# Kernel optimization log

Measured on AMD Instinct MI355X. Metric: run time of the kernel, lower is better.

## Reference

```python
import jax, jax.numpy as jnp
import numpy as np

# --- model hyperparams (match init_kwargs) ---
N_DIM = 200      # n_dim == nfeat == nhidden (Linear(200,200) hardcoded in source)
NHID = 200
NLAYERS = 8
ALPHA = 0.1
LAMDA = 0.5
B, L = 20, 100   # dialogues x uniform dialogue length
N = B * L        # 2000 utterances per modality -> 3N = 6000 graph nodes
A_DIM, V_DIM, L_DIM, NSPK = 300, 342, 1024, 2


def _linear_params(key, fin, fout):
    s = 1.0 / np.sqrt(fin)
    k1, k2 = jax.random.split(key)
    W = jax.random.uniform(k1, (fin, fout), jnp.float32, -s, s)
    b = jax.random.uniform(k2, (fout,), jnp.float32, -s, s)
    return W, b


def setup_inputs() -> dict:
    key = jax.random.key(0)
    ks = jax.random.split(key, 12)
    a = jax.random.normal(ks[0], (N, A_DIM), jnp.float32)
    v = jax.random.normal(ks[1], (N, V_DIM), jnp.float32)
    l = jax.random.normal(ks[2], (N, L_DIM), jnp.float32)
    qmask = jax.random.uniform(ks[3], (L, B, NSPK), dtype=jnp.float32)
    # dense normalized adjacency over the 3N-node multimodal graph
    adj = jax.random.uniform(ks[4], (3 * N, 3 * N), dtype=jnp.float32) / (3.0 * N)
    Wa, ba = _linear_params(ks[5], A_DIM, N_DIM)
    Wv, bv = _linear_params(ks[6], V_DIM, N_DIM)
    Wl, bl = _linear_params(ks[7], L_DIM, N_DIM)
    spk_emb = jax.random.normal(ks[8], (NSPK, N_DIM), jnp.float32)
    W0, b0 = _linear_params(ks[9], N_DIM, NHID)
    s = 1.0 / np.sqrt(NHID)
    # variant=True -> conv weight is [2*nhidden, nhidden]
    convW = jax.random.uniform(ks[10], (NLAYERS, 2 * NHID, NHID), jnp.float32, -s, s)
    return dict(a=a, v=v, l=l, qmask=qmask, adj=adj,
                Wa=Wa, ba=ba, Wv=Wv, bv=bv, Wl=Wl, bl=bl,
                spk_emb=spk_emb, W0=W0, b0=b0, convW=convW, dia_len=L)


def reference(a, v, l, qmask, adj, Wa, ba, Wv, bv, Wl, bl, spk_emb, W0, b0, convW, dia_len):
    # modality projections
    a = a @ Wa + ba                                   # [N, n_dim]
    v = v @ Wv + bv
    l = l @ Wl + bl
    # qmask: [L, B, n_spk] seq-first -> concat per dialogue (uniform lengths)
    qcat = jnp.transpose(qmask[:dia_len], (1, 0, 2)).reshape(-1, qmask.shape[-1])  # [N, n_spk]
    spk_idx = jnp.argmax(qcat, axis=-1)
    l = l + spk_emb[spk_idx]                          # use_speaker, 'l' in modals
    # big multimodal graph: stack modalities along node axis
    x = jnp.concatenate([a, v, l], axis=0)            # [3N, n_dim]
    # GCNII_lyc (eval mode: dropout identity)
    h0 = jax.nn.relu(x @ W0 + b0)                     # [3N, nhidden]
    thetas = jnp.log(LAMDA / jnp.arange(1, NLAYERS + 1, dtype=jnp.float32) + 1.0)

    def layer(h, wt):
        W, theta = wt
        hi = adj @ h                                  # spmm (dense here)
        support = jnp.concatenate([hi, h0], axis=1)   # variant=True
        r = (1.0 - ALPHA) * hi + ALPHA * h0
        h_new = jax.nn.relu(theta * (support @ W) + (1.0 - theta) * r)
        return h_new, None

    h, _ = jax.lax.scan(layer, h0, (convW, thetas))
    feat = jnp.concatenate([x, h], axis=1)            # use_residue -> [3N, n_dim+nhidden]
    n = a.shape[0]
    # split modality chunks back and fuse on feature axis -> [N, 3*(n_dim+nhidden)]
    return jnp.concatenate([feat[:n], feat[n:2 * n], feat[2 * n:3 * n]], axis=-1)
```

## Files before the change

### kernel.cpp

```cpp
#include <hip/hip_runtime.h>
#include <math.h>

typedef unsigned short u16;
typedef unsigned int u32;
typedef __bf16 bf8_t __attribute__((ext_vector_type(8)));
typedef float f4_t __attribute__((ext_vector_type(4)));
typedef u16 us8_t __attribute__((ext_vector_type(8)));
typedef u16 us4_t __attribute__((ext_vector_type(4)));

#define LDC 224
#define NROWS 6016
#define PLANE (NROWS*LDC)

__device__ __forceinline__ float b2f(u16 x){
  union{u32 u; float f;} c; c.u = ((u32)x)<<16; return c.f;
}
__device__ __forceinline__ u16 f2b(float f){
  union{u32 u; float f;} c; c.f = f;
  u32 b = c.u;
  return (u16)((b + 0x7FFFu + ((b>>16)&1u)) >> 16);
}
__device__ __forceinline__ u16 ldcvt(const void* p, size_t i, int f){
  return f ? f2b(((const float*)p)[i]) : ((const u16*)p)[i];
}

__global__ void detect_kernel(const u16* __restrict__ adj, int* __restrict__ flag)
{
  int l = threadIdx.x;
  u16 u = adj[2*l];
  int ex = (u >> 7) & 0xFF;
  bool ok = ((u >> 15) == 0) && (ex >= 0x30) && (ex <= 0x72);
  unsigned long long m = __ballot(ok);
  if (l == 0) flag[0] = (__popcll(m) < 32) ? 1 : 0;
}

__global__ void conv_kernel(const int* __restrict__ flag, const void* __restrict__ adj,
                            u16* __restrict__ adj_bf)
{
  const int f = flag[0];
  size_t idx = (size_t)blockIdx.x*256 + threadIdx.x;
  if (idx >= (size_t)6016*752) return;
  int row = (int)(idx / 752);
  int k8  = (int)(idx - (size_t)row*752) * 8;
  us8_t vv;
  if (row < 6000){
    if (f){
      const float* src = (const float*)adj + (size_t)row*6000;
      if (k8 + 8 <= 6000){
        f4_t x0 = *(const f4_t*)(src + k8);
        f4_t x1 = *(const f4_t*)(src + k8 + 4);
        #pragma unroll
        for (int j=0;j<4;j++){ vv[j] = f2b(x0[j]); vv[4+j] = f2b(x1[j]); }
      } else {
        #pragma unroll
        for (int j=0;j<8;j++){ int k=k8+j; vv[j] = (k<6000) ? f2b(src[k]) : (u16)0; }
      }
    } else {
      const u16* src = (const u16*)adj + (size_t)row*6000;
      if (k8 + 8 <= 6000){
        vv = *(const us8_t*)(src + k8);
      } else {
        #pragma unroll
        for (int j=0;j<8;j++){ int k=k8+j; vv[j] = (k<6000) ? src[k] : (u16)0; }
      }
    }
  } else {
    #pragma unroll
    for (int j=0;j<8;j++) vv[j] = 0;
  }
  *(us8_t*)(adj_bf + (size_t)row*6016 + k8) = vv;
}

__global__ void prep_kernel(const int* __restrict__ flag,
                            const void* __restrict__ Wa, const void* __restrict__ Wv,
                            const void* __restrict__ Wl, const void* __restrict__ W0,
                            const void* __restrict__ convW, const void* __restrict__ qmask,
                            const void* __restrict__ a_in, const void* __restrict__ v_in,
                            const void* __restrict__ l_in, const void* __restrict__ spkemb_in,
                            const void* __restrict__ ba, const void* __restrict__ bv,
                            const void* __restrict__ bl, const void* __restrict__ b0,
                            u16* __restrict__ WaT, u16* __restrict__ WvT, u16* __restrict__ WlT,
                            u16* __restrict__ W0T, u16* __restrict__ WtT, u16* __restrict__ WbT,
                            int* __restrict__ spk, u16* __restrict__ x_bf,
                            u16* __restrict__ a_p, u16* __restrict__ v_p, u16* __restrict__ l_p,
                            u16* __restrict__ spkem, u16* __restrict__ b_all)
{
  const int f = flag[0];
  const int y = blockIdx.y;
  const int e = blockIdx.x*256 + threadIdx.x;

  if (y < 20){
    const void* src; u16* dst; int K, kpad; size_t soff = 0;
    if (y == 0){ src=Wa; dst=WaT; K=300; kpad=320; }
    else if (y == 1){ src=Wv; dst=WvT; K=342; kpad=384; }
    else if (y == 2){ src=Wl; dst=WlT; K=1024; kpad=1024; }
    else if (y == 3){ src=W0; dst=W0T; K=200; kpad=256; }
    else if (y < 12){ int i=y-4;  src=convW; soff=(size_t)i*80000;          dst=WtT + i*57344; K=200; kpad=256; }
    else            { int i=y-12; src=convW; soff=(size_t)i*80000 + 40000;  dst=WbT + i*57344; K=200; kpad=256; }
    int total = 224*kpad;
    if (e >= total) return;
    int n = e / kpad, k = e - n*kpad;
    u16 val = 0;
    if (k < K && n < 200) val = ldcvt(src, soff + (size_t)k*200 + n, f);
    dst[e] = val;
    return;
  }
  if (y == 20){
    if (e < 2000){
      int b = e/100, t = e - b*100;
      size_t base = ((size_t)t*20 + b)*2;
      bool one;
      if (f) one = ((const float*)qmask)[base+1] > ((const float*)qmask)[base];
      else   one = b2f(((const u16*)qmask)[base+1]) > b2f(((const u16*)qmask)[base]);
      spk[e] = one ? 1 : 0;
    } else if (e < 2400){
      spkem[e-2000] = ldcvt(spkemb_in, e-2000, f);
    } else if (e < 3200){
      int j = e - 2400; int which = j/200, idx = j - which*200;
      const void* src = (which==0)?ba:(which==1)?bv:(which==2)?bl:b0;
      b_all[j] = ldcvt(src, idx, f);
    }
    return;
  }
  if (y == 21){
    if (e < 16*LDC) x_bf[(size_t)6000*LDC + e] = 0;
    return;
  }
  if (y < 25){
    size_t eg = (size_t)(y-22)*229376 + e;
    if (eg >= (size_t)2048*320) return;
    int row = (int)(eg/320), k = (int)(eg - (size_t)row*320);
    a_p[eg] = (row < 2000 && k < 300) ? ldcvt(a_in, (size_t)row*300 + k, f) : (u16)0;
    return;
  }
  if (y < 29){
    size_t eg = (size_t)(y-25)*229376 + e;
    if (eg >= (size_t)2048*384) return;
    int row = (int)(eg/384), k = (int)(eg - (size_t)row*384);
    v_p[eg] = (row < 2000 && k < 342) ? ldcvt(v_in, (size_t)row*342 + k, f) : (u16)0;
    return;
  }
  {
    size_t eg = (size_t)(y-29)*229376 + e;
    if (eg >= (size_t)2048*1024) return;
    int row = (int)(eg >> 10), k = (int)(eg & 1023);
    l_p[eg] = (row < 2000) ? ldcvt(l_in, (size_t)row*1024 + k, f) : (u16)0;
  }
}

__global__ __launch_bounds__(256, 2)
void gemm_kernel(const int* __restrict__ flag, int dynA,
                 const void* __restrict__ A1, int lda1, int kv1, int ks1, const u16* __restrict__ B1, int ldb1,
                 const u16* __restrict__ A2, int lda2, int kv2, int ks2, const u16* __restrict__ B2, int ldb2,
                 int Mv, int Mout, int spp, int emode,
                 const u16* __restrict__ bias, const u16* __restrict__ spk_e, const int* __restrict__ spk_idx,
                 u16* __restrict__ part_base,
                 const u16* __restrict__ hi_ro, const u16* __restrict__ h0_ro,
                 float theta,
                 u16* __restrict__ outN, u16* __restrict__ outT)
{
  __shared__ u16 ldsA[64*64];
  __shared__ u16 ldsB[224*64];
  const int fval = dynA ? flag[0] : 0;
  const int tid = threadIdx.x;
  const int l = tid & 63;
  const int w = tid >> 6;
  const int wrow = w >> 1, wcol = w & 1;
  const int row0 = blockIdx.x * 64;
  const int lq = l >> 4, lr = l & 15;

  f4_t acc[2][7];
  #pragma unroll
  for (int i=0;i<2;i++)
    #pragma unroll
    for (int j=0;j<7;j++){ f4_t z = {0.f,0.f,0.f,0.f}; acc[i][j] = z; }

  #pragma unroll 1
  for (int pair = 0; pair < 2; ++pair){
    const u16* A16 = pair ? A2 : (const u16*)A1;
    const float* A32 = pair ? nullptr : (const float*)A1;
    const int af32 = pair ? 0 : fval;
    int lda = pair ? lda2 : lda1;
    int kv = pair ? kv2 : kv1;      int ks = pair ? ks2 : ks1;
    const u16* B = pair ? B2 : B1;  int ldb = pair ? ldb2 : ldb1;
    int sb, se;
    if (pair == 0){ sb = blockIdx.y * spp; se = sb + spp; if (se > ks) se = ks; }
    else { sb = 0; se = ks; }

    #pragma unroll 1
    for (int s = sb; s < se; ++s){
      int k0 = s << 6;
      __syncthreads();
      bool fastA = ((lda & 7) == 0) && (row0 + 64 <= Mv) && (k0 + 64 <= kv);
      if (fastA){
        if (af32){
          const float* ap = A32 + (size_t)row0*lda + k0;
          #pragma unroll
          for (int i=0;i<2;i++){
            int c = tid + (i<<8);
            int m = c >> 3, k8 = c & 7;
            f4_t x0 = *(const f4_t*)(ap + (size_t)m*lda + (k8<<3));
            f4_t x1 = *(const f4_t*)(ap + (size_t)m*lda + (k8<<3) + 4);
            us8_t vv;
            #pragma unroll
            for (int j=0;j<4;j++){ vv[j] = f2b(x0[j]); vv[4+j] = f2b(x1[j]); }
            *(us8_t*)(&ldsA[(m<<6) + ((k8 ^ (m&7))<<3)]) = vv;
          }
        } else {
          const u16* ap = A16 + (size_t)row0*lda + k0;
          #pragma unroll
          for (int i=0;i<2;i++){
            int c = tid + (i<<8);
            int m = c >> 3, k8 = c & 7;
            us8_t vv = *(const us8_t*)(ap + (size_t)m*lda + (k8<<3));
            *(us8_t*)(&ldsA[(m<<6) + ((k8 ^ (m&7))<<3)]) = vv;
          }
        }
      } else {
        #pragma unroll
        for (int i=0;i<2;i++){
          int c = tid + (i<<8);
          int m = c >> 3, k8 = c & 7;
          int gr = row0 + m; if (gr > Mv-1) gr = Mv-1;
          us8_t vv;
          #pragma unroll
          for (int j=0;j<8;j++){
            int kk = k0 + (k8<<3) + j;
            u16 t = 0;
            if (kk < kv){
              if (af32) t = f2b(A32[(size_t)gr*lda + kk]);
              else      t = A16[(size_t)gr*lda + kk];
            }
            vv[j] = t;
          }
          *(us8_t*)(&ldsA[(m<<6) + ((k8 ^ (m&7))<<3)]) = vv;
        }
      }
      {
        const u16* bp = B + k0;
        #pragma unroll
        for (int i=0;i<7;i++){
          int c = tid + (i<<8);
          int n = c >> 3, k8 = c & 7;
          us8_t vv = *(const us8_t*)(bp + (size_t)n*ldb + (k8<<3));
          *(us8_t*)(&ldsB[(n<<6) + ((k8 ^ (n&7))<<3)]) = vv;
        }
      }
      __syncthreads();
      #pragma unroll
      for (int h=0; h<2; ++h){
        bf8_t af[2], bfr[7];
        int kc = lq + (h<<2);
        #pragma unroll
        for (int rt=0;rt<2;rt++){
          int m = wrow*32 + rt*16 + lr;
          af[rt] = *(const bf8_t*)(&ldsA[(m<<6) + ((kc ^ (m&7))<<3)]);
        }
        #pragma unroll
        for (int ct=0;ct<7;ct++){
          int n = wcol*112 + ct*16 + lr;
          bfr[ct] = *(const bf8_t*)(&ldsB[(n<<6) + ((kc ^ (n&7))<<3)]);
        }
        #pragma unroll
        for (int rt=0;rt<2;rt++)
          #pragma unroll
          for (int ct=0;ct<7;ct++)
            acc[rt][ct] = __builtin_amdgcn_mfma_f32_16x16x32_bf16(af[rt], bfr[ct], acc[rt][ct], 0,0,0);
      }
    }
  }

  #pragma unroll
  for (int rt=0;rt<2;rt++){
    int r_base = row0 + wrow*32 + rt*16 + lq*4;
    #pragma unroll
    for (int ct=0;ct<7;ct++){
      int c = wcol*112 + ct*16 + lr;
      f4_t a4 = acc[rt][ct];
      if (emode == 0){
        u16* dst = part_base + (size_t)blockIdx.y * PLANE;
        #pragma unroll
        for (int r=0;r<4;r++) dst[(size_t)(r_base+r)*LDC + c] = f2b(a4[r]);
      } else if (emode == 1){
        float bval = (c < 200) ? b2f(bias[c]) : 0.f;
        #pragma unroll
        for (int r=0;r<4;r++){
          int R = r_base + r;
          if (R < Mout){
            float vv = a4[r] + bval;
            if (spk_e && c < 200) vv += b2f(spk_e[spk_idx[R]*200 + c]);
            outN[(size_t)R*LDC + c] = f2b(vv);
          }
        }
      } else if (emode == 2){
        float bval = (c < 200) ? b2f(bias[c]) : 0.f;
        us4_t p;
        #pragma unroll
        for (int r=0;r<4;r++){
          int R = r_base + r;
          float vv = a4[r] + bval; if (vv < 0.f) vv = 0.f;
          u16 q = f2b(vv);
          outN[(size_t)R*LDC + c] = q;
          p[r] = q;
        }
        *(us4_t*)(&outT[(size_t)c*NROWS + r_base]) = p;
      } else {
        us4_t p;
        #pragma unroll
        for (int r=0;r<4;r++){
          int R = r_base + r;
          size_t ix = (size_t)R*LDC + c;
          float hiv = b2f(hi_ro[ix]), h0v = b2f(h0_ro[ix]);
          float rr = 0.9f*hiv + 0.1f*h0v;
          float vv = theta*a4[r] + (1.f - theta)*rr;
          if (vv < 0.f) vv = 0.f;
          p[r] = f2b(vv);
        }
        *(us4_t*)(&outT[(size_t)c*NROWS + r_base]) = p;
      }
    }
  }
}

__global__ void reduce_kernel(const u16* __restrict__ part, int nsk, u16* __restrict__ hi_bf)
{
  size_t i4 = ((size_t)blockIdx.x*256 + threadIdx.x)*4;
  float s0=0.f, s1=0.f, s2=0.f, s3=0.f;
  for (int p=0;p<nsk;p++){
    us4_t v = *(const us4_t*)(part + (size_t)p*PLANE + i4);
    s0 += b2f(v[0]); s1 += b2f(v[1]); s2 += b2f(v[2]); s3 += b2f(v[3]);
  }
  us4_t o; o[0]=f2b(s0); o[1]=f2b(s1); o[2]=f2b(s2); o[3]=f2b(s3);
  *(us4_t*)(hi_bf + i4) = o;
}

__device__ __forceinline__ u16 sent(u16 t, u16 snan, u16 sbig){
  u16 mag = t & 0x7FFF;
  if (mag >= 0x7F80) return snan;
  if (mag >= 0x4480) return sbig;
  return t;
}
__global__ void out_kernel(const int* __restrict__ flag,
                           const u16* __restrict__ x_bf, const u16* __restrict__ hT,
                           void* __restrict__ outp)
{
  __shared__ u16 tile[64*216];
  const int of32 = flag[0];
  u16* o16 = (u16*)outp;
  float* o32 = (float*)outp;
  const int tid = threadIdx.x;
  const int n0 = blockIdx.x*64;
  for (int m=0;m<3;m++){
    for (int cc = tid; cc < 1600; cc += 256){
      int r = cc/25, c8 = cc - r*25;
      int n = n0 + r;
      int rr = n < 2000 ? n : 1999;
      us8_t vv = *(const us8_t*)(x_bf + ((size_t)(m*2000 + rr))*LDC + c8*8);
      #pragma unroll
      for (int j=0;j<8;j++) vv[j] = sent(vv[j], 0x46EA, 0x46DB);
      if (n < 2000){
        size_t off = (size_t)n*1200 + m*400 + c8*8;
        if (!of32) *(us8_t*)(o16 + off) = vv;
        else {
          f4_t lo, hi;
          #pragma unroll
          for (int j=0;j<4;j++){ lo[j] = b2f(vv[j]); hi[j] = b2f(vv[4+j]); }
          *(f4_t*)(o32 + off) = lo; *(f4_t*)(o32 + off + 4) = hi;
        }
      }
    }
    __syncthreads();
    for (int cc = tid; cc < 1600; cc += 256){
      int c = cc >> 3, ng = cc & 7;
      int nb = n0 + ng*8;
      if (nb > 1992) nb = 1992;
      us8_t vv = *(const us8_t*)(hT + (size_t)c*NROWS + m*2000 + nb);
      #pragma unroll
      for (int j=0;j<8;j++) tile[(ng*8+j)*216 + c] = sent(vv[j], 0x469C, 0x468C);
    }
    __syncthreads();
    for (int cc = tid; cc < 1600; cc += 256){
      int r = cc/25, c8 = cc - r*25;
      int n = n0 + r;
      if (n < 2000){
        us8_t vv = *(const us8_t*)(&tile[r*216 + c8*8]);
        size_t off = (size_t)n*1200 + m*400 + 200 + c8*8;
        if (!of32) *(us8_t*)(o16 + off) = vv;
        else {
          f4_t lo, hi;
          #pragma unroll
          for (int j=0;j<4;j++){ lo[j] = b2f(vv[j]); hi[j] = b2f(vv[4+j]); }
          *(f4_t*)(o32 + off) = lo; *(f4_t*)(o32 + off + 4) = hi;
        }
      }
    }
    __syncthreads();
  }
}

extern "C" void kernel_launch(void* const* d_in, const int* in_sizes, int n_in,
                              void* d_out, int out_size, void* d_ws, size_t ws_size,
                              hipStream_t stream)
{
  const void* a     = d_in[0];
  const void* v     = d_in[1];
  const void* l     = d_in[2];
  const void* qmask = d_in[3];
  const void* adj   = d_in[4];
  const void* Wa    = d_in[5];
  const void* ba    = d_in[6];
  const void* Wv    = d_in[7];
  const void* bv    = d_in[8];
  const void* Wl    = d_in[9];
  const void* bl    = d_in[10];
  const void* spk_emb = d_in[11];
  const void* W0    = d_in[12];
  const void* b0    = d_in[13];
  const void* convW = d_in[14];

  int cfg = (ws_size >= (size_t)125*1024*1024) ? 2
          : (ws_size >= (size_t)48*1024*1024) ? 1 : 0;
  const int SK = (cfg >= 1) ? 8 : 2;
  const int SPP = (94 + SK - 1) / SK;

  char* ws = (char*)d_ws;
  size_t off = 0;
  auto alloc = [&](size_t bytes)->char*{
    char* p = ws + off; off = (off + bytes + 255) & ~(size_t)255; return p;
  };
  int*  flag  = (int*) alloc(256);
  u16*  x_bf  = (u16*) alloc((size_t)PLANE*2);
  u16*  h0_bf = (u16*) alloc((size_t)PLANE*2);
  u16*  hi_bf = (u16*) alloc((size_t)PLANE*2);
  u16*  hT    = (u16*) alloc((size_t)PLANE*2);
  u16*  a_p   = (u16*) alloc((size_t)2048*320*2);
  u16*  v_p   = (u16*) alloc((size_t)2048*384*2);
  u16*  l_p   = (u16*) alloc((size_t)2048*1024*2);
  u16* WaT = (u16*)alloc(224*320*2);
  u16* WvT = (u16*)alloc(224*384*2);
  u16* WlT = (u16*)alloc(224*1024*2);
  u16* W0T = (u16*)alloc(224*256*2);
  u16* WtT = (u16*)alloc((size_t)8*224*256*2);
  u16* WbT = (u16*)alloc((size_t)8*224*256*2);
  int* spk = (int*)alloc(2000*4);
  u16* spkem = (u16*)alloc(400*2);
  u16* b_all = (u16*)alloc(800*2);
  u16* part = (u16*)alloc((size_t)SK*PLANE*2);
  u16* adj_bf = (cfg == 2) ? (u16*)alloc((size_t)6016*6016*2) : nullptr;

  detect_kernel<<<1,64,0,stream>>>((const u16*)adj, flag);

  if (cfg == 2)
    conv_kernel<<<dim3(17672),256,0,stream>>>(flag, adj, adj_bf);

  prep_kernel<<<dim3(896,39),256,0,stream>>>(flag, Wa,Wv,Wl,W0,convW,qmask,
      a,v,l,spk_emb, ba,bv,bl,b0,
      WaT,WvT,WlT,W0T,WtT,WbT, spk, x_bf, a_p,v_p,l_p, spkem, b_all);

  gemm_kernel<<<dim3(32,1),256,0,stream>>>(flag,0, a_p,320,320,5, WaT,320,
      nullptr,0,0,0,nullptr,0, 2048,2000, 5, 1, b_all, nullptr, nullptr,
      nullptr, nullptr, nullptr, 0.f, x_bf, nullptr);
  gemm_kernel<<<dim3(32,1),256,0,stream>>>(flag,0, v_p,384,384,6, WvT,384,
      nullptr,0,0,0,nullptr,0, 2048,2000, 6, 1, b_all+200, nullptr, nullptr,
      nullptr, nullptr, nullptr, 0.f, x_bf + (size_t)2000*LDC, nullptr);
  gemm_kernel<<<dim3(32,1),256,0,stream>>>(flag,0, l_p,1024,1024,16, WlT,1024,
      nullptr,0,0,0,nullptr,0, 2048,2000, 16, 1, b_all+400, spkem, spk,
      nullptr, nullptr, nullptr, 0.f, x_bf + (size_t)4000*LDC, nullptr);

  gemm_kernel<<<dim3(94,1),256,0,stream>>>(flag,0, x_bf,LDC,LDC,4, W0T,256,
      nullptr,0,0,0,nullptr,0, NROWS,NROWS, 4, 2, b_all+600, nullptr, nullptr,
      nullptr, nullptr, nullptr, 0.f, h0_bf, hT);

  for (int i=0;i<8;i++){
    float theta = logf(0.5f/(float)(i+1) + 1.0f);
    if (cfg == 2)
      gemm_kernel<<<dim3(94,SK),256,0,stream>>>(flag,0, adj_bf,6016,6016,94, hT,NROWS,
          nullptr,0,0,0,nullptr,0, 6016,0, SPP, 0, nullptr, nullptr, nullptr,
          part, nullptr, nullptr, 0.f, nullptr, nullptr);
    else
      gemm_kernel<<<dim3(94,SK),256,0,stream>>>(flag,1, adj,6000,6000,94, hT,NROWS,
          nullptr,0,0,0,nullptr,0, 6000,0, SPP, 0, nullptr, nullptr, nullptr,
          part, nullptr, nullptr, 0.f, nullptr, nullptr);
    reduce_kernel<<<dim3(PLANE/1024),256,0,stream>>>(part, SK, hi_bf);
    gemm_kernel<<<dim3(94,1),256,0,stream>>>(flag,0, hi_bf,LDC,LDC,4, WtT + (size_t)i*57344,256,
        h0_bf,LDC,LDC,4, WbT + (size_t)i*57344,256,
        NROWS,0, 4, 3, nullptr, nullptr, nullptr, nullptr, hi_bf, h0_bf, theta,
        nullptr, hT);
  }

  out_kernel<<<dim3(32),256,0,stream>>>(flag, x_bf, hT, (void*)d_out);
}
```

Baseline: 767.5 us.

## Load GEMM tiles via direct global-to-LDS loads and template the row-tile height

Replaces the register-staged global→LDS copies for bf16 A and all B tiles with global_load_lds 16-byte direct loads, keeping the XOR swizzle by precomputing swizzled source addresses. The GEMM is templated on rows per warp (WR), so the small projection and per-layer GEMMs use 32-row tiles with twice as many blocks for better occupancy, while the adjacency GEMM keeps 64 rows. The reduce kernel is widened to 8 elements per thread. Risks include correctness around the new kg bound when reading padded columns, and the absence of explicit vmcnt waits before the barrier for the direct LDS loads.

```diff
diff --git a/kernel.cpp b/kernel.cpp
--- a/kernel.cpp
+++ b/kernel.cpp
@@ -22,6 +22,10 @@
 }
 __device__ __forceinline__ u16 ldcvt(const void* p, size_t i, int f){
   return f ? f2b(((const float*)p)[i]) : ((const u16*)p)[i];
+}
+__device__ __forceinline__ void gl16(const u16* g, u16* l){
+  __builtin_amdgcn_global_load_lds((const __attribute__((address_space(1))) void*)g,
+                                   (__attribute__((address_space(3))) void*)l, 16, 0, 0);
 }
 
 __global__ void detect_kernel(const u16* __restrict__ adj, int* __restrict__ flag)
@@ -148,10 +152,11 @@
   }
 }
 
+template<int WR>
 __global__ __launch_bounds__(256, 2)
 void gemm_kernel(const int* __restrict__ flag, int dynA,
-                 const void* __restrict__ A1, int lda1, int kv1, int ks1, const u16* __restrict__ B1, int ldb1,
-                 const u16* __restrict__ A2, int lda2, int kv2, int ks2, const u16* __restrict__ B2, int ldb2,
+                 const void* __restrict__ A1, int lda1, int kv1, int kg1, int ks1, const u16* __restrict__ B1, int ldb1,
+                 const u16* __restrict__ A2, int lda2, int kv2, int kg2, int ks2, const u16* __restrict__ B2, int ldb2,
                  int Mv, int Mout, int spp, int emode,
                  const u16* __restrict__ bias, const u16* __restrict__ spk_e, const int* __restrict__ spk_idx,
                  u16* __restrict__ part_base,
@@ -159,19 +164,19 @@
                  float theta,
                  u16* __restrict__ outN, u16* __restrict__ outT)
 {
-  __shared__ u16 ldsA[64*64];
+  __shared__ u16 ldsA[WR*32*64];
   __shared__ u16 ldsB[224*64];
   const int fval = dynA ? flag[0] : 0;
   const int tid = threadIdx.x;
   const int l = tid & 63;
   const int w = tid >> 6;
   const int wrow = w >> 1, wcol = w & 1;
-  const int row0 = blockIdx.x * 64;
+  const int row0 = blockIdx.x * (WR*32);
   const int lq = l >> 4, lr = l & 15;
 
-  f4_t acc[2][7];
+  f4_t acc[WR][7];
   #pragma unroll
-  for (int i=0;i<2;i++)
+  for (int i=0;i<WR;i++)
     #pragma unroll
     for (int j=0;j<7;j++){ f4_t z = {0.f,0.f,0.f,0.f}; acc[i][j] = z; }
 
@@ -182,6 +187,7 @@
     const int af32 = pair ? 0 : fval;
     int lda = pair ? lda2 : lda1;
     int kv = pair ? kv2 : kv1;      int ks = pair ? ks2 : ks1;
+    int kg = pair ? kg2 : kg1;
     const u16* B = pair ? B2 : B1;  int ldb = pair ? ldb2 : ldb1;
     int sb, se;
     if (pair == 0){ sb = blockIdx.y * spp; se = sb + spp; if (se > ks) se = ks; }
@@ -191,35 +197,34 @@
     for (int s = sb; s < se; ++s){
       int k0 = s << 6;
       __syncthreads();
-      bool fastA = ((lda & 7) == 0) && (row0 + 64 <= Mv) && (k0 + 64 <= kv);
-      if (fastA){
-        if (af32){
-          const float* ap = A32 + (size_t)row0*lda + k0;
+      bool alignedA = ((lda & 7) == 0) && (row0 + WR*32 <= Mv);
+      bool gldsA = (!af32) && alignedA && (k0 + 64 <= kg);
+      if (gldsA){
+        const u16* abase = A16 + k0;
+        #pragma unroll
+        for (int i=0;i<WR;i++){
+          int c = (i<<8) + tid;
+          int m = c >> 3, k8p = c & 7;
+          int k8 = k8p ^ (m & 7);
+          gl16(abase + (size_t)(row0+m)*lda + (k8<<3), &ldsA[c<<3]);
+        }
+      } else if (af32 && alignedA && (k0 + 64 <= kv)){
+        const float* ap = A32 + (size_t)row0*lda + k0;
+        #pragma unroll
+        for (int i=0;i<WR;i++){
+          int c = (i<<8) + tid;
+          int m = c >> 3, k8 = c & 7;
+          f4_t x0 = *(const f4_t*)(ap + (size_t)m*lda + (k8<<3));
+          f4_t x1 = *(const f4_t*)(ap + (size_t)m*lda + (k8<<3) + 4);
+          us8_t vv;
           #pragma unroll
-          for (int i=0;i<2;i++){
-            int c = tid + (i<<8);
-            int m = c >> 3, k8 = c & 7;
-            f4_t x0 = *(const f4_t*)(ap + (size_t)m*lda + (k8<<3));
-            f4_t x1 = *(const f4_t*)(ap + (size_t)m*lda + (k8<<3) + 4);
-            us8_t vv;
-            #pragma unroll
-            for (int j=0;j<4;j++){ vv[j] = f2b(x0[j]); vv[4+j] = f2b(x1[j]); }
-            *(us8_t*)(&ldsA[(m<<6) + ((k8 ^ (m&7))<<3)]) = vv;
-          }
-        } else {
-          const u16* ap = A16 + (size_t)row0*lda + k0;
-          #pragma unroll
-          for (int i=0;i<2;i++){
-            int c = tid + (i<<8);
-            int m = c >> 3, k8 = c & 7;
-            us8_t vv = *(const us8_t*)(ap + (size_t)m*lda + (k8<<3));
-            *(us8_t*)(&ldsA[(m<<6) + ((k8 ^ (m&7))<<3)]) = vv;
-          }
+          for (int j=0;j<4;j++){ vv[j] = f2b(x0[j]); vv[4+j] = f2b(x1[j]); }
+          *(us8_t*)(&ldsA[(m<<6) + ((k8 ^ (m&7))<<3)]) = vv;
         }
       } else {
         #pragma unroll
-        for (int i=0;i<2;i++){
-          int c = tid + (i<<8);
+        for (int i=0;i<WR;i++){
+          int c = (i<<8) + tid;
           int m = c >> 3, k8 = c & 7;
           int gr = row0 + m; if (gr > Mv-1) gr = Mv-1;
           us8_t vv;
@@ -237,23 +242,23 @@
         }
       }
       {
-        const u16* bp = B + k0;
+        const u16* bbase = B + k0;
         #pragma unroll
         for (int i=0;i<7;i++){
-          int c = tid + (i<<8);
-          int n = c >> 3, k8 = c & 7;
-          us8_t vv = *(const us8_t*)(bp + (size_t)n*ldb + (k8<<3));
-          *(us8_t*)(&ldsB[(n<<6) + ((k8 ^ (n&7))<<3)]) = vv;
+          int c = (i<<8) + tid;
+          int n = c >> 3, k8p = c & 7;
+          int k8 = k8p ^ (n & 7);
+          gl16(bbase + (size_t)n*ldb + (k8<<3), &ldsB[c<<3]);
         }
       }
       __syncthreads();
       #pragma unroll
       for (int h=0; h<2; ++h){
-        bf8_t af[2], bfr[7];
+        bf8_t af[WR], bfr[7];
         int kc = lq + (h<<2);
         #pragma unroll
-        for (int rt=0;rt<2;rt++){
-          int m = wrow*32 + rt*16 + lr;
+        for (int rt=0;rt<WR;rt++){
+          int m = wrow*(16*WR) + rt*16 + lr;
           af[rt] = *(const bf8_t*)(&ldsA[(m<<6) + ((kc ^ (m&7))<<3)]);
         }
         #pragma unroll
@@ -262,7 +267,7 @@
           bfr[ct] = *(const bf8_t*)(&ldsB[(n<<6) + ((kc ^ (n&7))<<3)]);
         }
         #pragma unroll
-        for (int rt=0;rt<2;rt++)
+        for (int rt=0;rt<WR;rt++)
           #pragma unroll
           for (int ct=0;ct<7;ct++)
             acc[rt][ct] = __builtin_amdgcn_mfma_f32_16x16x32_bf16(af[rt], bfr[ct], acc[rt][ct], 0,0,0);
@@ -271,8 +276,8 @@
   }
 
   #pragma unroll
-  for (int rt=0;rt<2;rt++){
-    int r_base = row0 + wrow*32 + rt*16 + lq*4;
+  for (int rt=0;rt<WR;rt++){
+    int r_base = row0 + wrow*(16*WR) + rt*16 + lq*4;
     #pragma unroll
     for (int ct=0;ct<7;ct++){
       int c = wcol*112 + ct*16 + lr;
@@ -324,14 +329,19 @@
 
 __global__ void reduce_kernel(const u16* __restrict__ part, int nsk, u16* __restrict__ hi_bf)
 {
-  size_t i4 = ((size_t)blockIdx.x*256 + threadIdx.x)*4;
-  float s0=0.f, s1=0.f, s2=0.f, s3=0.f;
+  size_t i8 = ((size_t)blockIdx.x*256 + threadIdx.x)*8;
+  float s[8];
+  #pragma unroll
+  for (int j=0;j<8;j++) s[j] = 0.f;
   for (int p=0;p<nsk;p++){
-    us4_t v = *(const us4_t*)(part + (size_t)p*PLANE + i4);
-    s0 += b2f(v[0]); s1 += b2f(v[1]); s2 += b2f(v[2]); s3 += b2f(v[3]);
-  }
-  us4_t o; o[0]=f2b(s0); o[1]=f2b(s1); o[2]=f2b(s2); o[3]=f2b(s3);
-  *(us4_t*)(hi_bf + i4) = o;
+    us8_t v = *(const us8_t*)(part + (size_t)p*PLANE + i8);
+    #pragma unroll
+    for (int j=0;j<8;j++) s[j] += b2f(v[j]);
+  }
+  us8_t o;
+  #pragma unroll
+  for (int j=0;j<8;j++) o[j] = f2b(s[j]);
+  *(us8_t*)(hi_bf + i8) = o;
 }
 
 __device__ __forceinline__ u16 sent(u16 t, u16 snan, u16 sbig){
@@ -457,33 +467,33 @@
       a,v,l,spk_emb, ba,bv,bl,b0,
       WaT,WvT,WlT,W0T,WtT,WbT, spk, x_bf, a_p,v_p,l_p, spkem, b_all);
 
-  gemm_kernel<<<dim3(32,1),256,0,stream>>>(flag,0, a_p,320,320,5, WaT,320,
-      nullptr,0,0,0,nullptr,0, 2048,2000, 5, 1, b_all, nullptr, nullptr,
+  gemm_kernel<1><<<dim3(64,1),256,0,stream>>>(flag,0, a_p,320,320,320,5, WaT,320,
+      nullptr,0,0,0,0,nullptr,0, 2048,2000, 5, 1, b_all, nullptr, nullptr,
       nullptr, nullptr, nullptr, 0.f, x_bf, nullptr);
-  gemm_kernel<<<dim3(32,1),256,0,stream>>>(flag,0, v_p,384,384,6, WvT,384,
-      nullptr,0,0,0,nullptr,0, 2048,2000, 6, 1, b_all+200, nullptr, nullptr,
+  gemm_kernel<1><<<dim3(64,1),256,0,stream>>>(flag,0, v_p,384,384,384,6, WvT,384,
+      nullptr,0,0,0,0,nullptr,0, 2048,2000, 6, 1, b_all+200, nullptr, nullptr,
       nullptr, nullptr, nullptr, 0.f, x_bf + (size_t)2000*LDC, nullptr);
-  gemm_kernel<<<dim3(32,1),256,0,stream>>>(flag,0, l_p,1024,1024,16, WlT,1024,
-      nullptr,0,0,0,nullptr,0, 2048,2000, 16, 1, b_all+400, spkem, spk,
+  gemm_kernel<1><<<dim3(64,1),256,0,stream>>>(flag,0, l_p,1024,1024,1024,16, WlT,1024,
+      nullptr,0,0,0,0,nullptr,0, 2048,2000, 16, 1, b_all+400, spkem, spk,
       nullptr, nullptr, nullptr, 0.f, x_bf + (size_t)4000*LDC, nullptr);
 
-  gemm_kernel<<<dim3(94,1),256,0,stream>>>(flag,0, x_bf,LDC,LDC,4, W0T,256,
-      nullptr,0,0,0,nullptr,0, NROWS,NROWS, 4, 2, b_all+600, nullptr, nullptr,
+  gemm_kernel<1><<<dim3(188,1),256,0,stream>>>(flag,0, x_bf,LDC,LDC,256,4, W0T,256,
+      nullptr,0,0,0,0,nullptr,0, NROWS,NROWS, 4, 2, b_all+600, nullptr, nullptr,
       nullptr, nullptr, nullptr, 0.f, h0_bf, hT);
 
   for (int i=0;i<8;i++){
     float theta = logf(0.5f/(float)(i+1) + 1.0f);
     if (cfg == 2)
-      gemm_kernel<<<dim3(94,SK),256,0,stream>>>(flag,0, adj_bf,6016,6016,94, hT,NROWS,
-          nullptr,0,0,0,nullptr,0, 6016,0, SPP, 0, nullptr, nullptr, nullptr,
+      gemm_kernel<2><<<dim3(94,SK),256,0,stream>>>(flag,0, adj_bf,6016,6016,6016,94, hT,NROWS,
+          nullptr,0,0,0,0,nullptr,0, 6016,0, SPP, 0, nullptr, nullptr, nullptr,
           part, nullptr, nullptr, 0.f, nullptr, nullptr);
     else
-      gemm_kernel<<<dim3(94,SK),256,0,stream>>>(flag,1, adj,6000,6000,94, hT,NROWS,
-          nullptr,0,0,0,nullptr,0, 6000,0, SPP, 0, nullptr, nullptr, nullptr,
+      gemm_kernel<2><<<dim3(94,SK),256,0,stream>>>(flag,1, adj,6000,6000,0,94, hT,NROWS,
+          nullptr,0,0,0,0,nullptr,0, 6000,0, SPP, 0, nullptr, nullptr, nullptr,
           part, nullptr, nullptr, 0.f, nullptr, nullptr);
-    reduce_kernel<<<dim3(PLANE/1024),256,0,stream>>>(part, SK, hi_bf);
-    gemm_kernel<<<dim3(94,1),256,0,stream>>>(flag,0, hi_bf,LDC,LDC,4, WtT + (size_t)i*57344,256,
-        h0_bf,LDC,LDC,4, WbT + (size_t)i*57344,256,
+    reduce_kernel<<<dim3(PLANE/2048),256,0,stream>>>(part, SK, hi_bf);
+    gemm_kernel<1><<<dim3(188,1),256,0,stream>>>(flag,0, hi_bf,LDC,LDC,256,4, WtT + (size_t)i*57344,256,
+        h0_bf,LDC,LDC,256,4, WbT + (size_t)i*57344,256,
         NROWS,0, 4, 3, nullptr, nullptr, nullptr, nullptr, hi_bf, h0_bf, theta,
         nullptr, hT);
   }
```

After: 734.7 us. 4.3% less time.
